# Kernel optimization log

Hardware: AMD Instinct MI355X
Metric: run time of the kernel (lower is better)

## Reference

```python
import jax, jax.numpy as jnp
import numpy as np

B, NL, C, H, W = 4, 2048, 128, 128, 128
N_PTS0, N_PTS1 = 32, 8
SCALE = N_PTS0 // N_PTS1  # MaxPool1d kernel/stride
FEATURE_DIM = 5
BN_EPS = 1e-5


def setup_inputs() -> dict:
    key = jax.random.key(0)
    ks = jax.random.split(key, 12)
    fm = jax.random.normal(ks[0], (B, C, H, W), dtype=jnp.float32)
    lines = jax.random.uniform(ks[1], (B, NL, 2, 2), dtype=jnp.float32) * 128.0
    P = C // 2
    s = 0.05
    return {
        "feature_map": fm,
        "lines": lines,
        # Bottleneck1D params (BatchNorm in eval mode: running_mean=0, running_var=1)
        "bn1_g": jnp.ones((C,), jnp.float32), "bn1_b": jnp.zeros((C,), jnp.float32),
        "conv1_w": jax.random.normal(ks[2], (P, C, 1), jnp.float32) * s,
        "conv1_b": jnp.zeros((P,), jnp.float32),
        "bn2_g": jnp.ones((P,), jnp.float32), "bn2_b": jnp.zeros((P,), jnp.float32),
        "conv2_w": jax.random.normal(ks[3], (P, P, 3), jnp.float32) * s,
        "conv2_b": jnp.zeros((P,), jnp.float32),
        "bn3_g": jnp.ones((P,), jnp.float32), "bn3_b": jnp.zeros((P,), jnp.float32),
        "conv3_w": jax.random.normal(ks[4], (C, P, 1), jnp.float32) * s,
        "conv3_b": jnp.zeros((C,), jnp.float32),
        # fc2: ReLU -> Linear(dim_loi*n_pts1 + 5, 4)
        "fc2_w": jax.random.normal(ks[5], (4, C * N_PTS1 + FEATURE_DIM), jnp.float32) * s,
        "fc2_b": jnp.zeros((4,), jnp.float32),
    }


def _bn(x, g, b):
    # eval-mode BatchNorm1d with running_mean=0, running_var=1
    return x * (g / jnp.sqrt(1.0 + BN_EPS))[None, :, None] + b[None, :, None]


def _conv1d(x, w, b, pad):
    y = jax.lax.conv_general_dilated(x, w, (1,), [(pad, pad)],
                                     dimension_numbers=("NCH", "OIH", "NCH"))
    return y + b[None, :, None]


def _loi_gather(fm, lines):
    # sample points along each line: [B, NL, N_PTS0, 2]
    lam = jnp.linspace(0.0, 1.0, N_PTS0, dtype=jnp.float32)[None, None, :, None]
    p = lines[:, :, 0:1, :] * lam + lines[:, :, 1:2, :] * (1.0 - lam) - 0.5
    p = p.reshape(B, -1, 2)                      # [B, NL*N_PTS0, 2]
    px, py = p[..., 0], p[..., 1]
    px0 = jnp.clip(jnp.floor(px), 0.0, 127.0)
    py0 = jnp.clip(jnp.floor(py), 0.0, 127.0)
    px1 = jnp.clip(px0 + 1.0, 0.0, 127.0)
    py1 = jnp.clip(py0 + 1.0, 0.0, 127.0)
    px0l, py0l = px0.astype(jnp.int32), py0.astype(jnp.int32)
    px1l, py1l = px1.astype(jnp.int32), py1.astype(jnp.int32)

    gather = jax.vmap(lambda f, yi, xi: f[:, yi, xi])  # [C, P] per image
    # weights exactly as in the torch source
    xp = (gather(fm, py0l, px0l) * ((px1 - px) * (py1 - py))[:, None, :]
          + gather(fm, py1l, px0l) * ((px - px0) * (py1 - py))[:, None, :]
          + gather(fm, py0l, px1l) * ((px1 - px) * (py - py0))[:, None, :]
          + gather(fm, py1l, px1l) * ((px - px0) * (py - py0))[:, None, :])
    # [B, C, NL*N_PTS0] -> [B*NL, C, N_PTS0]
    xp = xp.reshape(B, C, NL, N_PTS0).transpose(0, 2, 1, 3).reshape(B * NL, C, N_PTS0)
    return xp


def reference(feature_map, lines, bn1_g, bn1_b, conv1_w, conv1_b,
              bn2_g, bn2_b, conv2_w, conv2_b, bn3_g, bn3_b,
              conv3_w, conv3_b, fc2_w, fc2_b):
    xp = _loi_gather(feature_map, lines)               # [B*NL, C, N_PTS0]
    # MaxPool1d(SCALE, SCALE)
    x = xp.reshape(B * NL, C, N_PTS1, SCALE).max(axis=-1)
    # Bottleneck1D residual block
    y = jax.nn.relu(_bn(x, bn1_g, bn1_b))
    y = _conv1d(y, conv1_w, conv1_b, 0)
    y = jax.nn.relu(_bn(y, bn2_g, bn2_b))
    y = _conv1d(y, conv2_w, conv2_b, 1)
    y = jax.nn.relu(_bn(y, bn3_g, bn3_b))
    y = _conv1d(y, conv3_w, conv3_b, 0)
    x = x + y                                          # [B*NL, C, N_PTS1]
    # line geometry feature (use_cood=1, use_slop=1)
    xyu, xyv = lines[:, :, 0, :], lines[:, :, 1, :]
    u2v = jnp.sqrt(((xyu - xyv) ** 2).sum(-1, keepdims=True)).clip(min=1e-6)
    f = jnp.concatenate([xyu / 128.0, xyv / 128.0, u2v], axis=-1)
    f = f.reshape(B * NL, FEATURE_DIM)
    # concat + fc2 (ReLU -> Linear)
    x = jnp.concatenate([x.reshape(B * NL, C * N_PTS1), f], axis=1)
    logits = jax.nn.relu(x) @ fc2_w.T + fc2_b
    prob = jax.nn.softmax(logits, axis=1)
    return logits, prob
```

## Files before the change

kernel.cpp:

```cpp
#include <hip/hip_runtime.h>
#include <math.h>

#define BB 4
#define NLL 2048
#define CC 128
#define HH 128
#define WW 128
#define NPTS0 32
#define NPTS1 8
#define PP 64
#define FDIM 5
#define FCK (CC*NPTS1 + FDIM)

typedef __attribute__((ext_vector_type(8))) short bf16x8;
typedef __attribute__((ext_vector_type(4))) float f32x4;

__device__ __forceinline__ unsigned short f2bf(float f) {
    union { float f; unsigned u; } v; v.f = f;
    unsigned u = v.u;
    return (unsigned short)((u + 0x7fffu + ((u >> 16) & 1u)) >> 16);
}
__device__ __forceinline__ float bf2f(unsigned short s) {
    union { unsigned u; float f; } v; v.u = ((unsigned)s) << 16;
    return v.f;
}

__global__ __launch_bounds__(256)
void transpose_fm3(const float* __restrict__ fm, unsigned short* __restrict__ fmT) {
    __shared__ unsigned short tile[128 * 72];
    const int by = blockIdx.x >> 1;
    const int xh = blockIdx.x & 1;
    const int b = by >> 7, y = by & 127;
    const int t = threadIdx.x;
    const float* src = fm + ((size_t)b * CC) * (HH * WW) + (size_t)y * WW + xh * 64;
    const int x4 = (t & 15) * 4;
    const int r0 = t >> 4;
    #pragma unroll
    for (int i = 0; i < 8; ++i) {
        int r = r0 + 16 * i;
        float4 v = *(const float4*)&src[(size_t)r * (HH * WW) + x4];
        ushort4 u;
        u.x = f2bf(v.x); u.y = f2bf(v.y); u.z = f2bf(v.z); u.w = f2bf(v.w);
        *(ushort4*)&tile[r * 72 + (x4 ^ (r & 28))] = u;
    }
    __syncthreads();
    unsigned short* dst = fmT + ((size_t)by * WW + xh * 64) * CC;
    const int c4 = (t & 31) * 4;
    #pragma unroll
    for (int i = 0; i < 8; ++i) {
        int x = (t >> 5) + 8 * i;
        ushort4 u;
        u.x = tile[(c4 + 0) * 72 + (x ^ ((c4 + 0) & 28))];
        u.y = tile[(c4 + 1) * 72 + (x ^ ((c4 + 1) & 28))];
        u.z = tile[(c4 + 2) * 72 + (x ^ ((c4 + 2) & 28))];
        u.w = tile[(c4 + 3) * 72 + (x ^ ((c4 + 3) & 28))];
        *(ushort4*)&dst[(size_t)x * CC + c4] = u;
    }
}

__global__ __launch_bounds__(256)
void prep_weights(const float* __restrict__ w1, const float* __restrict__ w2,
                  const float* __restrict__ w3, unsigned short* __restrict__ W1b,
                  unsigned short* __restrict__ W2b, unsigned short* __restrict__ W3b) {
    int gid = blockIdx.x * 256 + threadIdx.x;
    if (gid < 8192) {
        W1b[gid] = f2bf(w1[gid]);
    } else if (gid < 20480) {
        int g = gid - 8192;
        int tt = g >> 12, r = g & 4095;
        int p = r >> 6, q = r & 63;
        W2b[tt * 4096 + p * 64 + q] = f2bf(w2[p * 192 + q * 3 + tt]);
    } else if (gid < 28672) {
        int g = gid - 20480;
        W3b[g] = f2bf(w3[g]);
    }
}

__global__ __launch_bounds__(256)
void line_mfma(const unsigned short* __restrict__ fmT,
               const float* __restrict__ lines,
               const float* __restrict__ bn1_g, const float* __restrict__ bn1_b,
               const unsigned short* __restrict__ W1b, const float* __restrict__ b1,
               const float* __restrict__ bn2_g, const float* __restrict__ bn2_b,
               const unsigned short* __restrict__ W2b, const float* __restrict__ b2,
               const float* __restrict__ bn3_g, const float* __restrict__ bn3_b,
               const unsigned short* __restrict__ W3b, const float* __restrict__ b3,
               const float* __restrict__ fcw,   const float* __restrict__ fcb,
               float* __restrict__ out) {
    __shared__ int   s_oA[64], s_oB[64], s_oC[64], s_oD[64];
    __shared__ float s_wA[64], s_wB[64], s_wC[64], s_wD[64];
    __shared__ float s_xs[16 * 128];
    __shared__ unsigned short s_ybn[16 * 136];
    __shared__ unsigned short s_z1[2 * 10 * 72];
    __shared__ unsigned short s_z2[16 * 72];
    __shared__ float s_feat[2][8];
    __shared__ float s_red[4 * 8];

    const int bx  = blockIdx.x;
    const int L0  = bx * 2;
    const int b   = bx >> 10;
    const int tid = threadIdx.x;
    const int lane = tid & 63;
    const int wv   = tid >> 6;
    const int quad = lane >> 4;
    const int l16  = lane & 15;
    const float inv_s = 1.0f / sqrtf(1.0f + 1e-5f);

    if (tid < 64) {
        int line = tid >> 5, pt = tid & 31;
        const float* ln = lines + (size_t)(L0 + line) * 4;
        float lam = (float)pt * (1.0f / 31.0f);
        float om  = 1.0f - lam;
        float px = ln[0] * lam + ln[2] * om - 0.5f;
        float py = ln[1] * lam + ln[3] * om - 0.5f;
        float px0 = fminf(fmaxf(floorf(px), 0.0f), 127.0f);
        float py0 = fminf(fmaxf(floorf(py), 0.0f), 127.0f);
        float px1 = fminf(px0 + 1.0f, 127.0f);
        float py1 = fminf(py0 + 1.0f, 127.0f);
        int ix0 = (int)px0, ix1 = (int)px1, iy0 = (int)py0, iy1 = (int)py1;
        s_oA[tid] = (iy0 * WW + ix0) * CC;
        s_oB[tid] = (iy1 * WW + ix0) * CC;
        s_oC[tid] = (iy0 * WW + ix1) * CC;
        s_oD[tid] = (iy1 * WW + ix1) * CC;
        float ax = px1 - px, bxv = px - px0, ay = py1 - py, byv = py - py0;
        s_wA[tid] = ax  * ay;
        s_wB[tid] = bxv * ay;
        s_wC[tid] = ax  * byv;
        s_wD[tid] = bxv * byv;
    }
    if (tid >= 64 && tid < 66) {
        int line = tid - 64;
        const float* ln = lines + (size_t)(L0 + line) * 4;
        float ux = ln[0], uy = ln[1], vx = ln[2], vy = ln[3];
        float dx = ux - vx, dy = uy - vy;
        float d = fmaxf(sqrtf(dx * dx + dy * dy), 1e-6f);
        s_feat[line][0] = ux * (1.0f / 128.0f);
        s_feat[line][1] = uy * (1.0f / 128.0f);
        s_feat[line][2] = vx * (1.0f / 128.0f);
        s_feat[line][3] = vy * (1.0f / 128.0f);
        s_feat[line][4] = d;
    }
    if (tid < 128) {
        int line = tid >> 6, q = tid & 63;
        s_z1[line * 720 + 0 * 72 + q] = 0;
        s_z1[line * 720 + 9 * 72 + q] = 0;
    }
    __syncthreads();

    {
        int tl = tid >> 4;
        int line = tl >> 3, k = tl & 7;
        int c8 = (tid & 15) * 8;
        const unsigned short* base = fmT + (size_t)b * (HH * WW * CC) + c8;
        float acc[8];
        #pragma unroll
        for (int i = 0; i < 8; ++i) acc[i] = -INFINITY;
        #pragma unroll
        for (int j = 0; j < 4; ++j) {
            int pt = line * 32 + k * 4 + j;
            bf16x8 rA = *(const bf16x8*)(base + s_oA[pt]);
            bf16x8 rB = *(const bf16x8*)(base + s_oB[pt]);
            bf16x8 rC = *(const bf16x8*)(base + s_oC[pt]);
            bf16x8 rD = *(const bf16x8*)(base + s_oD[pt]);
            float wA = s_wA[pt], wB = s_wB[pt], wC = s_wC[pt], wD = s_wD[pt];
            #pragma unroll
            for (int i = 0; i < 8; ++i) {
                float v = wA * bf2f((unsigned short)rA[i])
                        + wB * bf2f((unsigned short)rB[i])
                        + wC * bf2f((unsigned short)rC[i])
                        + wD * bf2f((unsigned short)rD[i]);
                acc[i] = fmaxf(acc[i], v);
            }
        }
        float* xr = &s_xs[tl * 128 + c8];
        #pragma unroll
        for (int i = 0; i < 8; ++i) xr[i] = acc[i];
    }
    __syncthreads();

    {
        int m = tid >> 4, c8 = (tid & 15) * 8;
        const float* xr = &s_xs[m * 128 + c8];
        bf16x8 pack;
        #pragma unroll
        for (int i = 0; i < 8; ++i) {
            float v = fmaxf(xr[i] * (bn1_g[c8 + i] * inv_s) + bn1_b[c8 + i], 0.0f);
            pack[i] = (short)f2bf(v);
        }
        *(bf16x8*)&s_ybn[m * 136 + c8] = pack;
    }
    __syncthreads();

    {
        int n0 = wv * 16;
        f32x4 acc = {0.f, 0.f, 0.f, 0.f};
        #pragma unroll
        for (int kc = 0; kc < 4; ++kc) {
            bf16x8 a = *(const bf16x8*)&s_ybn[l16 * 136 + kc * 32 + quad * 8];
            bf16x8 bf = *(const bf16x8*)(W1b + (n0 + l16) * 128 + kc * 32 + quad * 8);
            acc = __builtin_amdgcn_mfma_f32_16x16x32_bf16(a, bf, acc, 0, 0, 0);
        }
        int p = n0 + l16;
        float s2 = bn2_g[p] * inv_s, bb2 = bn2_b[p], cb = b1[p];
        int line = quad >> 1;
        int kbase = (quad & 1) * 4;
        #pragma unroll
        for (int r = 0; r < 4; ++r) {
            float v = fmaxf((acc[r] + cb) * s2 + bb2, 0.0f);
            s_z1[line * 720 + (kbase + r + 1) * 72 + p] = f2bf(v);
        }
    }
    __syncthreads();

    {
        int n0 = wv * 16;
        f32x4 acc = {0.f, 0.f, 0.f, 0.f};
        int line = l16 >> 3, k = l16 & 7;
        #pragma unroll
        for (int t = 0; t < 3; ++t) {
            const unsigned short* arow = &s_z1[line * 720 + (k + t) * 72];
            #pragma unroll
            for (int kc = 0; kc < 2; ++kc) {
                bf16x8 a = *(const bf16x8*)&arow[kc * 32 + quad * 8];
                bf16x8 bf = *(const bf16x8*)(W2b + t * 4096 + (n0 + l16) * 64 + kc * 32 + quad * 8);
                acc = __builtin_amdgcn_mfma_f32_16x16x32_bf16(a, bf, acc, 0, 0, 0);
            }
        }
        int p = n0 + l16;
        float s3 = bn3_g[p] * inv_s, bb3 = bn3_b[p], cb = b2[p];
        #pragma unroll
        for (int r = 0; r < 4; ++r) {
            float v = fmaxf((acc[r] + cb) * s3 + bb3, 0.0f);
            s_z2[(quad * 4 + r) * 72 + p] = f2bf(v);
        }
    }
    __syncthreads();

    float p0 = 0.f, p1 = 0.f, p2 = 0.f, p3 = 0.f;
    {
        int kbase = (quad & 1) * 4;
        bf16x8 a0 = *(const bf16x8*)&s_z2[l16 * 72 + 0 * 32 + quad * 8];
        bf16x8 a1 = *(const bf16x8*)&s_z2[l16 * 72 + 1 * 32 + quad * 8];
        #pragma unroll
        for (int sub = 0; sub < 2; ++sub) {
            int n0 = wv * 32 + sub * 16;
            f32x4 acc = {0.f, 0.f, 0.f, 0.f};
            bf16x8 bf0 = *(const bf16x8*)(W3b + (n0 + l16) * 64 + 0 * 32 + quad * 8);
            bf16x8 bf1 = *(const bf16x8*)(W3b + (n0 + l16) * 64 + 1 * 32 + quad * 8);
            acc = __builtin_amdgcn_mfma_f32_16x16x32_bf16(a0, bf0, acc, 0, 0, 0);
            acc = __builtin_amdgcn_mfma_f32_16x16x32_bf16(a1, bf1, acc, 0, 0, 0);
            int c = n0 + l16;
            float cb = b3[c];
            #pragma unroll
            for (int r = 0; r < 4; ++r) {
                int m = quad * 4 + r;
                float v = fmaxf(s_xs[m * 128 + c] + acc[r] + cb, 0.0f);
                int idx = c * 8 + kbase + r;
                p0 = fmaf(v, fcw[0 * FCK + idx], p0);
                p1 = fmaf(v, fcw[1 * FCK + idx], p1);
                p2 = fmaf(v, fcw[2 * FCK + idx], p2);
                p3 = fmaf(v, fcw[3 * FCK + idx], p3);
            }
        }
    }
    #pragma unroll
    for (int off = 16; off >= 1; off >>= 1) {
        p0 += __shfl_down(p0, off);
        p1 += __shfl_down(p1, off);
        p2 += __shfl_down(p2, off);
        p3 += __shfl_down(p3, off);
    }
    if ((lane & 31) == 0) {
        int line = lane >> 5;
        s_red[wv * 8 + line * 4 + 0] = p0;
        s_red[wv * 8 + line * 4 + 1] = p1;
        s_red[wv * 8 + line * 4 + 2] = p2;
        s_red[wv * 8 + line * 4 + 3] = p3;
    }
    __syncthreads();

    if (tid < 2) {
        int line = tid;
        float lg[4];
        #pragma unroll
        for (int o = 0; o < 4; ++o) {
            lg[o] = fcb[o] + s_red[0 + line * 4 + o] + s_red[8 + line * 4 + o]
                  + s_red[16 + line * 4 + o] + s_red[24 + line * 4 + o];
        }
        #pragma unroll
        for (int j = 0; j < FDIM; ++j) {
            float fv = fmaxf(s_feat[line][j], 0.0f);
            #pragma unroll
            for (int o = 0; o < 4; ++o)
                lg[o] = fmaf(fv, fcw[o * FCK + 1024 + j], lg[o]);
        }
        float m = fmaxf(fmaxf(lg[0], lg[1]), fmaxf(lg[2], lg[3]));
        float e0 = expf(lg[0] - m), e1 = expf(lg[1] - m);
        float e2 = expf(lg[2] - m), e3 = expf(lg[3] - m);
        float inv = 1.0f / (e0 + e1 + e2 + e3);
        float* lo = out + (size_t)(L0 + line) * 4;
        lo[0] = lg[0]; lo[1] = lg[1]; lo[2] = lg[2]; lo[3] = lg[3];
        float* pr = out + (size_t)BB * NLL * 4 + (size_t)(L0 + line) * 4;
        pr[0] = e0 * inv; pr[1] = e1 * inv; pr[2] = e2 * inv; pr[3] = e3 * inv;
    }
}

__global__ __launch_bounds__(256)
void transpose_fm2(const float* __restrict__ fm, float* __restrict__ fmT) {
    __shared__ float tile[32 * 132];
    const int c0 = blockIdx.x * 32;
    const int by = blockIdx.y;
    const int b = by >> 7, y = by & 127;
    const int t = threadIdx.x;
    const float* src = fm + ((size_t)b * CC) * (HH * WW) + (size_t)y * WW;
    const int x4 = (t & 31) * 4;
    #pragma unroll
    for (int i = 0; i < 4; ++i) {
        int r = (t >> 5) + 8 * i;
        *(float4*)&tile[r * 132 + x4] =
            *(const float4*)&src[(size_t)(c0 + r) * (HH * WW) + x4];
    }
    __syncthreads();
    float* dst = fmT + (size_t)by * WW * CC + c0 + (t & 31);
    const int cr = (t & 31) * 132;
    #pragma unroll
    for (int i = 0; i < 16; ++i) {
        int x = (t >> 5) + 8 * i;
        dst[(size_t)x * CC] = tile[cr + x];
    }
}

template<bool TRANS>
__global__ __launch_bounds__(256)
void line_kernel_v1(const float* __restrict__ fm,
                    const float* __restrict__ lines,
                    const float* __restrict__ bn1_g, const float* __restrict__ bn1_b,
                    const float* __restrict__ w1,    const float* __restrict__ b1,
                    const float* __restrict__ bn2_g, const float* __restrict__ bn2_b,
                    const float* __restrict__ w2,    const float* __restrict__ b2,
                    const float* __restrict__ bn3_g, const float* __restrict__ bn3_b,
                    const float* __restrict__ w3,    const float* __restrict__ b3,
                    const float* __restrict__ fcw,   const float* __restrict__ fcb,
                    float* __restrict__ out) {
    __shared__ int   s_ix0[32], s_ix1[32], s_iy0[32], s_iy1[32];
    __shared__ float s_wA[32], s_wB[32], s_wC[32], s_wD[32];
    __shared__ float xs [8][132];
    __shared__ float ybn[8][132];
    __shared__ float z1 [64][12];
    __shared__ float z2 [64][8];
    __shared__ float s_feat[8];
    __shared__ float s_red[16];

    const int L   = blockIdx.x;
    const int b   = L / NLL;
    const int tid = threadIdx.x;
    const float inv_s = 1.0f / sqrtf(1.0f + 1e-5f);
    const float* ln = lines + (size_t)L * 4;

    if (tid < 32) {
        float lam = (float)tid * (1.0f / 31.0f);
        float om  = 1.0f - lam;
        float px = ln[0] * lam + ln[2] * om - 0.5f;
        float py = ln[1] * lam + ln[3] * om - 0.5f;
        float px0 = fminf(fmaxf(floorf(px), 0.0f), 127.0f);
        float py0 = fminf(fmaxf(floorf(py), 0.0f), 127.0f);
        float px1 = fminf(px0 + 1.0f, 127.0f);
        float py1 = fminf(py0 + 1.0f, 127.0f);
        s_ix0[tid] = (int)px0; s_ix1[tid] = (int)px1;
        s_iy0[tid] = (int)py0; s_iy1[tid] = (int)py1;
        float ax = px1 - px, bxv = px - px0, ay = py1 - py, byv = py - py0;
        s_wA[tid] = ax  * ay;  s_wB[tid] = bxv * ay;
        s_wC[tid] = ax  * byv; s_wD[tid] = bxv * byv;
    }
    if (tid == 0) {
        float ux = ln[0], uy = ln[1], vx = ln[2], vy = ln[3];
        float dx = ux - vx, dy = uy - vy;
        float d = fmaxf(sqrtf(dx * dx + dy * dy), 1e-6f);
        s_feat[0] = ux / 128.0f; s_feat[1] = uy / 128.0f;
        s_feat[2] = vx / 128.0f; s_feat[3] = vy / 128.0f;
        s_feat[4] = d;
    }
    __syncthreads();
    {
        int cq = tid & 31, k = tid >> 5, c0 = cq * 4;
        float4 acc;
        acc.x = -INFINITY; acc.y = -INFINITY; acc.z = -INFINITY; acc.w = -INFINITY;
        #pragma unroll
        for (int j = 0; j < 4; ++j) {
            int pt = k * 4 + j;
            int ix0 = s_ix0[pt], ix1 = s_ix1[pt];
            int iy0 = s_iy0[pt], iy1 = s_iy1[pt];
            float wA = s_wA[pt], wB = s_wB[pt], wC = s_wC[pt], wD = s_wD[pt];
            float4 vA, vB, vC, vD;
            if (TRANS) {
                const float* base = fm + (size_t)b * HH * WW * CC;
                vA = *(const float4*)(base + ((size_t)(iy0 * WW + ix0)) * CC + c0);
                vB = *(const float4*)(base + ((size_t)(iy1 * WW + ix0)) * CC + c0);
                vC = *(const float4*)(base + ((size_t)(iy0 * WW + ix1)) * CC + c0);
                vD = *(const float4*)(base + ((size_t)(iy1 * WW + ix1)) * CC + c0);
            } else {
                const float* base = fm + ((size_t)b * CC + c0) * HH * WW;
                int oA = iy0 * WW + ix0, oB = iy1 * WW + ix0;
                int oC = iy0 * WW + ix1, oD = iy1 * WW + ix1;
                vA.x = base[oA];           vB.x = base[oB];
                vC.x = base[oC];           vD.x = base[oD];
                vA.y = base[HH*WW + oA];   vB.y = base[HH*WW + oB];
                vC.y = base[HH*WW + oC];   vD.y = base[HH*WW + oD];
                vA.z = base[2*HH*WW + oA]; vB.z = base[2*HH*WW + oB];
                vC.z = base[2*HH*WW + oC]; vD.z = base[2*HH*WW + oD];
                vA.w = base[3*HH*WW + oA]; vB.w = base[3*HH*WW + oB];
                vC.w = base[3*HH*WW + oC]; vD.w = base[3*HH*WW + oD];
            }
            float4 v;
            v.x = wA * vA.x + wB * vB.x + wC * vC.x + wD * vD.x;
            v.y = wA * vA.y + wB * vB.y + wC * vC.y + wD * vD.y;
            v.z = wA * vA.z + wB * vB.z + wC * vC.z + wD * vD.z;
            v.w = wA * vA.w + wB * vB.w + wC * vC.w + wD * vD.w;
            acc.x = fmaxf(acc.x, v.x); acc.y = fmaxf(acc.y, v.y);
            acc.z = fmaxf(acc.z, v.z); acc.w = fmaxf(acc.w, v.w);
        }
        *(float4*)(&xs[k][c0]) = acc;
    }
    __syncthreads();
    for (int e = tid; e < 1024; e += 256) {
        int k = e >> 7, c = e & 127;
        ybn[k][c] = fmaxf(xs[k][c] * (bn1_g[c] * inv_s) + bn1_b[c], 0.0f);
    }
    __syncthreads();
    if (tid < 64) { z1[tid][0] = 0.0f; z1[tid][9] = 0.0f; }
    {
        int p = tid >> 2, kq = tid & 3;
        const float* wrow = w1 + p * 128;
        float a0a = 0.f, a0b = 0.f, a1a = 0.f, a1b = 0.f;
        #pragma unroll 8
        for (int c = 0; c < 128; c += 4) {
            float4 w  = *(const float4*)(wrow + c);
            float4 ya = *(const float4*)(&ybn[kq][c]);
            float4 yb = *(const float4*)(&ybn[kq + 4][c]);
            a0a = fmaf(w.x, ya.x, a0a); a0b = fmaf(w.y, ya.y, a0b);
            a0a = fmaf(w.z, ya.z, a0a); a0b = fmaf(w.w, ya.w, a0b);
            a1a = fmaf(w.x, yb.x, a1a); a1b = fmaf(w.y, yb.y, a1b);
            a1a = fmaf(w.z, yb.z, a1a); a1b = fmaf(w.w, yb.w, a1b);
        }
        float s2 = bn2_g[p] * inv_s, bb = bn2_b[p], cb = b1[p];
        z1[p][1 + kq]     = fmaxf((a0a + a0b + cb) * s2 + bb, 0.0f);
        z1[p][1 + kq + 4] = fmaxf((a1a + a1b + cb) * s2 + bb, 0.0f);
    }
    __syncthreads();
    {
        int p = tid >> 2, kq = tid & 3;
        const float* wrow = w2 + p * 192;
        float acc0 = 0.f, acc1 = 0.f;
        #pragma unroll 4
        for (int q = 0; q < 64; ++q) {
            float w0 = wrow[q * 3 + 0], w1v = wrow[q * 3 + 1], w2v = wrow[q * 3 + 2];
            const float* zr = &z1[q][0];
            acc0 = fmaf(w0, zr[kq], acc0);
            acc0 = fmaf(w1v, zr[kq + 1], acc0);
            acc0 = fmaf(w2v, zr[kq + 2], acc0);
            acc1 = fmaf(w0, zr[kq + 4], acc1);
            acc1 = fmaf(w1v, zr[kq + 5], acc1);
            acc1 = fmaf(w2v, zr[kq + 6], acc1);
        }
        float s3 = bn3_g[p] * inv_s, bb = bn3_b[p], cb = b2[p];
        z2[p][kq]     = fmaxf((acc0 + cb) * s3 + bb, 0.0f);
        z2[p][kq + 4] = fmaxf((acc1 + cb) * s3 + bb, 0.0f);
    }
    __syncthreads();
    float part0 = 0.f, part1 = 0.f, part2 = 0.f, part3 = 0.f;
    {
        int c = tid >> 1, kq = tid & 1;
        const float* wrow = w3 + c * 64;
        float acc[4] = {0.f, 0.f, 0.f, 0.f};
        #pragma unroll 8
        for (int q = 0; q < 64; ++q) {
            float w = wrow[q];
            acc[0] = fmaf(w, z2[q][kq], acc[0]);
            acc[1] = fmaf(w, z2[q][kq + 2], acc[1]);
            acc[2] = fmaf(w, z2[q][kq + 4], acc[2]);
            acc[3] = fmaf(w, z2[q][kq + 6], acc[3]);
        }
        float cb = b3[c];
        #pragma unroll
        for (int i = 0; i < 4; ++i) {
            int k = kq + 2 * i;
            float v = fmaxf(xs[k][c] + acc[i] + cb, 0.0f);
            int idx = c * 8 + k;
            part0 = fmaf(v, fcw[0 * FCK + idx], part0);
            part1 = fmaf(v, fcw[1 * FCK + idx], part1);
            part2 = fmaf(v, fcw[2 * FCK + idx], part2);
            part3 = fmaf(v, fcw[3 * FCK + idx], part3);
        }
    }
    #pragma unroll
    for (int off = 32; off > 0; off >>= 1) {
        part0 += __shfl_down(part0, off);
        part1 += __shfl_down(part1, off);
        part2 += __shfl_down(part2, off);
        part3 += __shfl_down(part3, off);
    }
    if ((tid & 63) == 0) {
        int w = tid >> 6;
        s_red[w * 4 + 0] = part0; s_red[w * 4 + 1] = part1;
        s_red[w * 4 + 2] = part2; s_red[w * 4 + 3] = part3;
    }
    __syncthreads();
    if (tid == 0) {
        float lg[4];
        #pragma unroll
        for (int o = 0; o < 4; ++o)
            lg[o] = fcb[o] + s_red[o] + s_red[4 + o] + s_red[8 + o] + s_red[12 + o];
        #pragma unroll
        for (int j = 0; j < FDIM; ++j) {
            float fv = fmaxf(s_feat[j], 0.0f);
            #pragma unroll
            for (int o = 0; o < 4; ++o)
                lg[o] = fmaf(fv, fcw[o * FCK + 1024 + j], lg[o]);
        }
        float m = fmaxf(fmaxf(lg[0], lg[1]), fmaxf(lg[2], lg[3]));
        float e0 = expf(lg[0] - m), e1 = expf(lg[1] - m);
        float e2 = expf(lg[2] - m), e3 = expf(lg[3] - m);
        float inv = 1.0f / (e0 + e1 + e2 + e3);
        float* lo = out + (size_t)L * 4;
        lo[0] = lg[0]; lo[1] = lg[1]; lo[2] = lg[2]; lo[3] = lg[3];
        float* pr = out + (size_t)BB * NLL * 4 + (size_t)L * 4;
        pr[0] = e0 * inv; pr[1] = e1 * inv; pr[2] = e2 * inv; pr[3] = e3 * inv;
    }
}

extern "C" void kernel_launch(void* const* d_in, const int* in_sizes, int n_in,
                              void* d_out, int out_size, void* d_ws, size_t ws_size,
                              hipStream_t stream) {
    const float* fm     = (const float*)d_in[0];
    const float* lines  = (const float*)d_in[1];
    const float* bn1_g  = (const float*)d_in[2];
    const float* bn1_b  = (const float*)d_in[3];
    const float* w1     = (const float*)d_in[4];
    const float* b1     = (const float*)d_in[5];
    const float* bn2_g  = (const float*)d_in[6];
    const float* bn2_b  = (const float*)d_in[7];
    const float* w2     = (const float*)d_in[8];
    const float* b2     = (const float*)d_in[9];
    const float* bn3_g  = (const float*)d_in[10];
    const float* bn3_b  = (const float*)d_in[11];
    const float* w3     = (const float*)d_in[12];
    const float* b3     = (const float*)d_in[13];
    const float* fcw    = (const float*)d_in[14];
    const float* fcb    = (const float*)d_in[15];
    float* out = (float*)d_out;

    const size_t fmTb_bytes = (size_t)BB * HH * WW * CC * sizeof(unsigned short);
    const size_t fmTf_bytes = (size_t)BB * HH * WW * CC * sizeof(float);
    const size_t wb_bytes   = 57344;

    if (ws_size >= fmTb_bytes + wb_bytes) {
        unsigned short* fmT = (unsigned short*)d_ws;
        unsigned short* W1b = (unsigned short*)((char*)d_ws + fmTb_bytes);
        unsigned short* W2b = W1b + 8192;
        unsigned short* W3b = W2b + 12288;
        prep_weights<<<112, 256, 0, stream>>>(w1, w2, w3, W1b, W2b, W3b);
        transpose_fm3<<<BB * HH * 2, 256, 0, stream>>>(fm, fmT);
        line_mfma<<<BB * NLL / 2, 256, 0, stream>>>(
            fmT, lines, bn1_g, bn1_b, W1b, b1, bn2_g, bn2_b, W2b, b2,
            bn3_g, bn3_b, W3b, b3, fcw, fcb, out);
    } else if (ws_size >= fmTf_bytes) {
        float* fmT = (float*)d_ws;
        dim3 tg(CC / 32, BB * HH);
        transpose_fm2<<<tg, 256, 0, stream>>>(fm, fmT);
        line_kernel_v1<true><<<BB * NLL, 256, 0, stream>>>(
            fmT, lines, bn1_g, bn1_b, w1, b1, bn2_g, bn2_b, w2, b2,
            bn3_g, bn3_b, w3, b3, fcw, fcb, out);
    } else {
        line_kernel_v1<false><<<BB * NLL, 256, 0, stream>>>(
            fm, lines, bn1_g, bn1_b, w1, b1, bn2_g, bn2_b, w2, b2,
            bn3_g, bn3_b, w3, b3, fcw, fcb, out);
    }
}
```

Measured before the change: 154.3 us.

## Fuse weight prep into transpose kernel, pad fc weights, drop a barrier

Merges the weight-conversion kernel into the feature-map transpose kernel, with extra blocks doing weight prep, and makes each transpose block handle a full row instead of half. Adds a padded copy of the fc2 weights so the fc epilogue can use float4 vector loads. Fuses the BN1/ReLU packing into the gather stage, removing one __syncthreads and an LDS round trip. Pads s_xs rows to 132 to avoid bank conflicts and adds an occupancy hint to launch_bounds. The cost is one fewer kernel launch, at the price of larger transpose blocks using more LDS and a little extra workspace.

```diff
diff --git a/kernel.cpp b/kernel.cpp
--- a/kernel.cpp
+++ b/kernel.cpp
@@ -11,6 +11,7 @@
 #define PP 64
 #define FDIM 5
 #define FCK (CC*NPTS1 + FDIM)
+#define FCKP 1032
 
 typedef __attribute__((ext_vector_type(8))) short bf16x8;
 typedef __attribute__((ext_vector_type(4))) float f32x4;
@@ -26,57 +27,69 @@
 }
 
 __global__ __launch_bounds__(256)
-void transpose_fm3(const float* __restrict__ fm, unsigned short* __restrict__ fmT) {
-    __shared__ unsigned short tile[128 * 72];
-    const int by = blockIdx.x >> 1;
-    const int xh = blockIdx.x & 1;
+void transpose_prep(const float* __restrict__ fm, const float* __restrict__ w1,
+                    const float* __restrict__ w2, const float* __restrict__ w3,
+                    const float* __restrict__ fcw,
+                    unsigned short* __restrict__ fmT,
+                    unsigned short* __restrict__ W1b,
+                    unsigned short* __restrict__ W2b,
+                    unsigned short* __restrict__ W3b,
+                    float* __restrict__ fcwP) {
+    const int t = threadIdx.x;
+    if (blockIdx.x >= 512) {
+        int gid = (blockIdx.x - 512) * 256 + t;
+        for (int e = gid; e < 32800; e += 4096) {
+            if (e < 8192) {
+                W1b[e] = f2bf(w1[e]);
+            } else if (e < 20480) {
+                int g = e - 8192;
+                int tt = g >> 12, r = g & 4095;
+                int p = r >> 6, q = r & 63;
+                W2b[tt * 4096 + p * 64 + q] = f2bf(w2[p * 192 + q * 3 + tt]);
+            } else if (e < 28672) {
+                int g = e - 20480;
+                W3b[g] = f2bf(w3[g]);
+            } else {
+                int g = e - 28672;
+                int o = g / FCKP, r = g - o * FCKP;
+                fcwP[g] = (r < FCK) ? fcw[o * FCK + r] : 0.0f;
+            }
+        }
+        return;
+    }
+    __shared__ unsigned short tile[2][128 * 72];
+    const int by = blockIdx.x;
     const int b = by >> 7, y = by & 127;
-    const int t = threadIdx.x;
-    const float* src = fm + ((size_t)b * CC) * (HH * WW) + (size_t)y * WW + xh * 64;
-    const int x4 = (t & 15) * 4;
-    const int r0 = t >> 4;
+    const float* src = fm + ((size_t)b * CC) * (HH * WW) + (size_t)y * WW;
+    const int x4 = (t & 31) * 4;
+    const int xh = x4 >> 6, xl = x4 & 63;
     #pragma unroll
-    for (int i = 0; i < 8; ++i) {
-        int r = r0 + 16 * i;
+    for (int i = 0; i < 16; ++i) {
+        int r = (t >> 5) + 8 * i;
         float4 v = *(const float4*)&src[(size_t)r * (HH * WW) + x4];
         ushort4 u;
         u.x = f2bf(v.x); u.y = f2bf(v.y); u.z = f2bf(v.z); u.w = f2bf(v.w);
-        *(ushort4*)&tile[r * 72 + (x4 ^ (r & 28))] = u;
-    }
-    __syncthreads();
-    unsigned short* dst = fmT + ((size_t)by * WW + xh * 64) * CC;
+        *(ushort4*)&tile[xh][r * 72 + (xl ^ (r & 28))] = u;
+    }
+    __syncthreads();
     const int c4 = (t & 31) * 4;
     #pragma unroll
-    for (int i = 0; i < 8; ++i) {
-        int x = (t >> 5) + 8 * i;
-        ushort4 u;
-        u.x = tile[(c4 + 0) * 72 + (x ^ ((c4 + 0) & 28))];
-        u.y = tile[(c4 + 1) * 72 + (x ^ ((c4 + 1) & 28))];
-        u.z = tile[(c4 + 2) * 72 + (x ^ ((c4 + 2) & 28))];
-        u.w = tile[(c4 + 3) * 72 + (x ^ ((c4 + 3) & 28))];
-        *(ushort4*)&dst[(size_t)x * CC + c4] = u;
-    }
-}
-
-__global__ __launch_bounds__(256)
-void prep_weights(const float* __restrict__ w1, const float* __restrict__ w2,
-                  const float* __restrict__ w3, unsigned short* __restrict__ W1b,
-                  unsigned short* __restrict__ W2b, unsigned short* __restrict__ W3b) {
-    int gid = blockIdx.x * 256 + threadIdx.x;
-    if (gid < 8192) {
-        W1b[gid] = f2bf(w1[gid]);
-    } else if (gid < 20480) {
-        int g = gid - 8192;
-        int tt = g >> 12, r = g & 4095;
-        int p = r >> 6, q = r & 63;
-        W2b[tt * 4096 + p * 64 + q] = f2bf(w2[p * 192 + q * 3 + tt]);
-    } else if (gid < 28672) {
-        int g = gid - 20480;
-        W3b[g] = f2bf(w3[g]);
-    }
-}
-
-__global__ __launch_bounds__(256)
+    for (int h = 0; h < 2; ++h) {
+        unsigned short* dst = fmT + ((size_t)by * WW + h * 64) * CC;
+        #pragma unroll
+        for (int i = 0; i < 8; ++i) {
+            int x = (t >> 5) + 8 * i;
+            ushort4 u;
+            u.x = tile[h][(c4 + 0) * 72 + (x ^ ((c4 + 0) & 28))];
+            u.y = tile[h][(c4 + 1) * 72 + (x ^ ((c4 + 1) & 28))];
+            u.z = tile[h][(c4 + 2) * 72 + (x ^ ((c4 + 2) & 28))];
+            u.w = tile[h][(c4 + 3) * 72 + (x ^ ((c4 + 3) & 28))];
+            *(ushort4*)&dst[(size_t)x * CC + c4] = u;
+        }
+    }
+}
+
+__global__ __launch_bounds__(256, 8)
 void line_mfma(const unsigned short* __restrict__ fmT,
                const float* __restrict__ lines,
                const float* __restrict__ bn1_g, const float* __restrict__ bn1_b,
@@ -85,11 +98,11 @@
                const unsigned short* __restrict__ W2b, const float* __restrict__ b2,
                const float* __restrict__ bn3_g, const float* __restrict__ bn3_b,
                const unsigned short* __restrict__ W3b, const float* __restrict__ b3,
-               const float* __restrict__ fcw,   const float* __restrict__ fcb,
+               const float* __restrict__ fcwP,  const float* __restrict__ fcb,
                float* __restrict__ out) {
     __shared__ int   s_oA[64], s_oB[64], s_oC[64], s_oD[64];
     __shared__ float s_wA[64], s_wB[64], s_wC[64], s_wD[64];
-    __shared__ float s_xs[16 * 128];
+    __shared__ float s_xs[16 * 132];
     __shared__ unsigned short s_ybn[16 * 136];
     __shared__ unsigned short s_z1[2 * 10 * 72];
     __shared__ unsigned short s_z2[16 * 72];
@@ -172,22 +185,18 @@
                 acc[i] = fmaxf(acc[i], v);
             }
         }
-        float* xr = &s_xs[tl * 128 + c8];
-        #pragma unroll
-        for (int i = 0; i < 8; ++i) xr[i] = acc[i];
-    }
-    __syncthreads();
-
-    {
-        int m = tid >> 4, c8 = (tid & 15) * 8;
-        const float* xr = &s_xs[m * 128 + c8];
+        float* xr = &s_xs[tl * 132 + c8];
+        f32x4 lo = {acc[0], acc[1], acc[2], acc[3]};
+        f32x4 hi = {acc[4], acc[5], acc[6], acc[7]};
+        *(f32x4*)&xr[0] = lo;
+        *(f32x4*)&xr[4] = hi;
         bf16x8 pack;
         #pragma unroll
         for (int i = 0; i < 8; ++i) {
-            float v = fmaxf(xr[i] * (bn1_g[c8 + i] * inv_s) + bn1_b[c8 + i], 0.0f);
+            float v = fmaxf(acc[i] * (bn1_g[c8 + i] * inv_s) + bn1_b[c8 + i], 0.0f);
             pack[i] = (short)f2bf(v);
         }
-        *(bf16x8*)&s_ybn[m * 136 + c8] = pack;
+        *(bf16x8*)&s_ybn[tl * 136 + c8] = pack;
     }
     __syncthreads();
 
@@ -251,15 +260,23 @@
             acc = __builtin_amdgcn_mfma_f32_16x16x32_bf16(a1, bf1, acc, 0, 0, 0);
             int c = n0 + l16;
             float cb = b3[c];
+            int idx = c * 8 + kbase;
+            float4 w0 = *(const float4*)(fcwP + 0 * FCKP + idx);
+            float4 w1v = *(const float4*)(fcwP + 1 * FCKP + idx);
+            float4 w2v = *(const float4*)(fcwP + 2 * FCKP + idx);
+            float4 w3v = *(const float4*)(fcwP + 3 * FCKP + idx);
+            const float* w0a = (const float*)&w0;
+            const float* w1a = (const float*)&w1v;
+            const float* w2a = (const float*)&w2v;
+            const float* w3a = (const float*)&w3v;
             #pragma unroll
             for (int r = 0; r < 4; ++r) {
                 int m = quad * 4 + r;
-                float v = fmaxf(s_xs[m * 128 + c] + acc[r] + cb, 0.0f);
-                int idx = c * 8 + kbase + r;
-                p0 = fmaf(v, fcw[0 * FCK + idx], p0);
-                p1 = fmaf(v, fcw[1 * FCK + idx], p1);
-                p2 = fmaf(v, fcw[2 * FCK + idx], p2);
-                p3 = fmaf(v, fcw[3 * FCK + idx], p3);
+                float v = fmaxf(s_xs[m * 132 + c] + acc[r] + cb, 0.0f);
+                p0 = fmaf(v, w0a[r], p0);
+                p1 = fmaf(v, w1a[r], p1);
+                p2 = fmaf(v, w2a[r], p2);
+                p3 = fmaf(v, w3a[r], p3);
             }
         }
     }
@@ -292,7 +309,7 @@
             float fv = fmaxf(s_feat[line][j], 0.0f);
             #pragma unroll
             for (int o = 0; o < 4; ++o)
-                lg[o] = fmaf(fv, fcw[o * FCK + 1024 + j], lg[o]);
+                lg[o] = fmaf(fv, fcwP[o * FCKP + 1024 + j], lg[o]);
         }
         float m = fmaxf(fmaxf(lg[0], lg[1]), fmaxf(lg[2], lg[3]));
         float e0 = expf(lg[0] - m), e1 = expf(lg[1] - m);
@@ -552,17 +569,19 @@
     const size_t fmTb_bytes = (size_t)BB * HH * WW * CC * sizeof(unsigned short);
     const size_t fmTf_bytes = (size_t)BB * HH * WW * CC * sizeof(float);
     const size_t wb_bytes   = 57344;
-
-    if (ws_size >= fmTb_bytes + wb_bytes) {
+    const size_t fcwP_bytes = 4 * FCKP * sizeof(float);
+
+    if (ws_size >= fmTb_bytes + wb_bytes + fcwP_bytes) {
         unsigned short* fmT = (unsigned short*)d_ws;
         unsigned short* W1b = (unsigned short*)((char*)d_ws + fmTb_bytes);
         unsigned short* W2b = W1b + 8192;
         unsigned short* W3b = W2b + 12288;
-        prep_weights<<<112, 256, 0, stream>>>(w1, w2, w3, W1b, W2b, W3b);
-        transpose_fm3<<<BB * HH * 2, 256, 0, stream>>>(fm, fmT);
+        float* fcwP = (float*)((char*)d_ws + fmTb_bytes + wb_bytes);
+        transpose_prep<<<512 + 16, 256, 0, stream>>>(
+            fm, w1, w2, w3, fcw, fmT, W1b, W2b, W3b, fcwP);
         line_mfma<<<BB * NLL / 2, 256, 0, stream>>>(
             fmT, lines, bn1_g, bn1_b, W1b, b1, bn2_g, bn2_b, W2b, b2,
-            bn3_g, bn3_b, W3b, b3, fcw, fcb, out);
+            bn3_g, bn3_b, W3b, b3, fcwP, fcb, out);
     } else if (ws_size >= fmTf_bytes) {
         float* fmT = (float*)d_ws;
         dim3 tg(CC / 32, BB * HH);
```

Result: faster. 149.8 us (-2.9%).
